# Kernel optimization log

Measured on AMD Instinct MI355X. Metric: run time of the kernel, lower is better.

## Reference

```python
import jax, jax.numpy as jnp
import numpy as np


def setup_inputs() -> dict:
    key = jax.random.key(0)
    ks = jax.random.split(key, 10)
    b, l, d, n, dc = 4, 4096, 768, 16, 4
    w = lambda k, shape, s: jax.random.normal(k, shape, jnp.float32) * s
    return {
        "x": w(ks[0], (b, l, d), 1.0),
        "state": jnp.zeros((b, d, n), jnp.float32),
        "W_in": w(ks[1], (d, 2 * d), 0.02),      # in_proj (expand_factor=2)
        "conv_w": w(ks[2], (d, dc), 0.1),          # depthwise conv1d weight [d_model, d_conv]
        "conv_b": w(ks[3], (d,), 0.02),
        "W_x": w(ks[4], (d, 2 * n), 0.02),         # x_proj -> (B, C)
        "W_dt": w(ks[5], (d, d), 0.02),
        "b_dt": w(ks[6], (d,), 0.02),
        "A_log": w(ks[7], (d, n), 0.1),
        "D": jnp.ones((d,), jnp.float32),
        "W_out": w(ks[8], (d, d), 0.02),
    }


def reference(x, state, W_in, conv_w, conv_b, W_x, W_dt, b_dt, A_log, D, W_out):
    b, l, d = x.shape
    n = A_log.shape[1]
    dc = conv_w.shape[1]

    xz = x @ W_in                              # [b,l,2d]
    x_ssm, z = jnp.split(xz, 2, axis=-1)       # each [b,l,d]

    # causal depthwise conv1d (torch pads by dc-1 both sides then truncates to l)
    xp = jnp.pad(x_ssm, ((0, 0), (dc - 1, 0), (0, 0)))
    x_conv = conv_b
    for k in range(dc):
        x_conv = x_conv + xp[:, k:k + l, :] * conv_w[:, k]
    x_ssm = jax.nn.silu(x_conv)

    A = -jnp.exp(A_log)                        # [d,n]
    dt = jax.nn.softplus(x_ssm @ W_dt + b_dt)  # [b,l,d]
    B_seq, C_seq = jnp.split(x_ssm @ W_x, 2, axis=-1)  # each [b,l,n]

    # selective scan: state[b,d,n] = state*exp(dt*A) + B*x ; y = <state,C> + D*x
    def step(s, inp):
        x_t, B_t, C_t, dt_t = inp              # [b,d],[b,n],[b,n],[b,d]
        dA = jnp.exp(dt_t[:, :, None] * A)     # [b,d,n]
        s = s * dA + B_t[:, None, :] * x_t[:, :, None]
        y = jnp.einsum('bdn,bn->bd', s, C_t) + D * x_t
        return s, y

    s0 = jnp.zeros((b, d, n), x.dtype)         # parallel_selective_scan starts from zeros
    _, ys = jax.lax.scan(
        step, s0,
        (x_ssm.transpose(1, 0, 2), B_seq.transpose(1, 0, 2),
         C_seq.transpose(1, 0, 2), dt.transpose(1, 0, 2)))
    y = ys.transpose(1, 0, 2)                  # [b,l,d]

    y = y * jax.nn.silu(z)
    out = y @ W_out
    # use_fused_ops path returns the (unchanged) incoming state as new_state
    return out, state
```

## Files before the change

kernel.cpp:

```cpp
#include <hip/hip_runtime.h>
#include <hip/hip_bf16.h>
#include <cstdint>
#include <cstddef>

constexpr int Bc = 4, Lc = 4096, Dc = 768, Nc = 16;
constexpr int M_TOT = Bc * Lc;
constexpr int NCH = 128;
constexpr int TCH = Lc / NCH;
constexpr int Kd = 768;
constexpr int TWO_D = 1536;

typedef __attribute__((ext_vector_type(8))) short short8v;
typedef __attribute__((ext_vector_type(4))) float f32x4;

__device__ __forceinline__ float fexp2(float x) {
#if __has_builtin(__builtin_amdgcn_exp2f)
    return __builtin_amdgcn_exp2f(x);
#else
    return exp2f(x);
#endif
}
__device__ __forceinline__ float softplusf(float x) {
    return (x > 20.0f) ? x : __logf(1.0f + __expf(x));
}
__device__ __forceinline__ float siluf(float x) {
    return x / (1.0f + __expf(-x));
}

__device__ __forceinline__ void swizzled_tile(int& row0, int& col0)
{
    const int nwg = gridDim.x * gridDim.y;
    const int bid = blockIdx.y * gridDim.x + blockIdx.x;
    const int swz = (bid & 7) * (nwg >> 3) + (bid >> 3);
    row0 = (swz / gridDim.x) * 128;
    col0 = (swz % gridDim.x) * 128;
}

__global__ __launch_bounds__(256)
void gemm_bf16_f32(const __hip_bfloat16* __restrict__ Ab,
                   const __hip_bfloat16* __restrict__ Wt,
                   int N, float* __restrict__ out0)
{
    __shared__ __hip_bfloat16 Asm[128 * 32];
    __shared__ __hip_bfloat16 Bsm[128 * 32];
    const int tid = threadIdx.x;
    const int w = tid >> 6, lane = tid & 63;
    const int lr = lane & 15, lc = lane >> 4;
    int row0, col0;
    swizzled_tile(row0, col0);
    const int wrow = (w >> 1) * 64, wcol = (w & 1) * 64;

    const int srow = lane >> 2;
    const int scol = (lane & 3) * 8;

    f32x4 acc[4][4] = {};

    const int KT = Kd / 32;
    for (int kt = 0; kt < KT; ++kt) {
        if (kt) __syncthreads();
        #pragma unroll
        for (int i = 0; i < 2; ++i) {
            const int seg = w * 2 + i;
            const __hip_bfloat16* asrc =
                Ab + (size_t)(row0 + seg * 16 + srow) * Kd + kt * 32 + scol;
            const __hip_bfloat16* bsrc =
                Wt + (size_t)(col0 + seg * 16 + srow) * Kd + kt * 32 + scol;
            __builtin_amdgcn_global_load_lds(
                (const __attribute__((address_space(1))) void*)asrc,
                (__attribute__((address_space(3))) void*)(Asm + seg * 512), 16, 0, 0);
            __builtin_amdgcn_global_load_lds(
                (const __attribute__((address_space(1))) void*)bsrc,
                (__attribute__((address_space(3))) void*)(Bsm + seg * 512), 16, 0, 0);
        }
        asm volatile("s_waitcnt vmcnt(0)" ::: "memory");
        __syncthreads();

        short8v a[4], b[4];
        #pragma unroll
        for (int m = 0; m < 4; ++m)
            a[m] = *(const short8v*)((char*)Asm + (wrow + m * 16 + lr) * 64 + lc * 16);
        #pragma unroll
        for (int nf = 0; nf < 4; ++nf)
            b[nf] = *(const short8v*)((char*)Bsm + (wcol + nf * 16 + lr) * 64 + lc * 16);
        #pragma unroll
        for (int m = 0; m < 4; ++m)
            #pragma unroll
            for (int nf = 0; nf < 4; ++nf)
                acc[m][nf] = __builtin_amdgcn_mfma_f32_16x16x32_bf16(
                    a[m], b[nf], acc[m][nf], 0, 0, 0);
    }

    #pragma unroll
    for (int m = 0; m < 4; ++m)
        #pragma unroll
        for (int nf = 0; nf < 4; ++nf)
            #pragma unroll
            for (int j = 0; j < 4; ++j) {
                const int rg = row0 + wrow + m * 16 + lc * 4 + j;
                const int cg = col0 + wcol + nf * 16 + lr;
                out0[(size_t)rg * N + cg] = acc[m][nf][j];
            }
}

__global__ __launch_bounds__(256)
void gemm_bf16_b16(const __hip_bfloat16* __restrict__ Ab,
                   const __hip_bfloat16* __restrict__ Wt,
                   int N, __hip_bfloat16* __restrict__ outb)
{
    __shared__ __hip_bfloat16 Asm[128 * 32];
    __shared__ __hip_bfloat16 Bsm[128 * 32];
    const int tid = threadIdx.x;
    const int w = tid >> 6, lane = tid & 63;
    const int lr = lane & 15, lc = lane >> 4;
    int row0, col0;
    swizzled_tile(row0, col0);
    const int wrow = (w >> 1) * 64, wcol = (w & 1) * 64;

    const int srow = lane >> 2;
    const int scol = (lane & 3) * 8;

    f32x4 acc[4][4] = {};

    const int KT = Kd / 32;
    for (int kt = 0; kt < KT; ++kt) {
        if (kt) __syncthreads();
        #pragma unroll
        for (int i = 0; i < 2; ++i) {
            const int seg = w * 2 + i;
            const __hip_bfloat16* asrc =
                Ab + (size_t)(row0 + seg * 16 + srow) * Kd + kt * 32 + scol;
            const __hip_bfloat16* bsrc =
                Wt + (size_t)(col0 + seg * 16 + srow) * Kd + kt * 32 + scol;
            __builtin_amdgcn_global_load_lds(
                (const __attribute__((address_space(1))) void*)asrc,
                (__attribute__((address_space(3))) void*)(Asm + seg * 512), 16, 0, 0);
            __builtin_amdgcn_global_load_lds(
                (const __attribute__((address_space(1))) void*)bsrc,
                (__attribute__((address_space(3))) void*)(Bsm + seg * 512), 16, 0, 0);
        }
        asm volatile("s_waitcnt vmcnt(0)" ::: "memory");
        __syncthreads();

        short8v a[4], b[4];
        #pragma unroll
        for (int m = 0; m < 4; ++m)
            a[m] = *(const short8v*)((char*)Asm + (wrow + m * 16 + lr) * 64 + lc * 16);
        #pragma unroll
        for (int nf = 0; nf < 4; ++nf)
            b[nf] = *(const short8v*)((char*)Bsm + (wcol + nf * 16 + lr) * 64 + lc * 16);
        #pragma unroll
        for (int m = 0; m < 4; ++m)
            #pragma unroll
            for (int nf = 0; nf < 4; ++nf)
                acc[m][nf] = __builtin_amdgcn_mfma_f32_16x16x32_bf16(
                    a[m], b[nf], acc[m][nf], 0, 0, 0);
    }

    #pragma unroll
    for (int m = 0; m < 4; ++m)
        #pragma unroll
        for (int nf = 0; nf < 4; ++nf)
            #pragma unroll
            for (int j = 0; j < 4; ++j) {
                const int rg = row0 + wrow + m * 16 + lc * 4 + j;
                const int cg = col0 + wcol + nf * 16 + lr;
                outb[(size_t)rg * N + cg] = __float2bfloat16(acc[m][nf][j]);
            }
}

__global__ __launch_bounds__(256)
void bc_mfma(const __hip_bfloat16* __restrict__ xsb,
             const __hip_bfloat16* __restrict__ WxT,
             float* __restrict__ BC)
{
    const int w = threadIdx.x >> 6, lane = threadIdx.x & 63;
    const int lr = lane & 15, lc = lane >> 4;
    const int row0 = blockIdx.x * 64 + w * 16;

    f32x4 acc0 = {}, acc1 = {};
    const __hip_bfloat16* ap = xsb + (size_t)(row0 + lr) * Kd + lc * 8;
    const __hip_bfloat16* b0p = WxT + (size_t)lr * Kd + lc * 8;
    const __hip_bfloat16* b1p = WxT + (size_t)(16 + lr) * Kd + lc * 8;
    #pragma unroll 4
    for (int kt = 0; kt < Kd / 32; ++kt) {
        const short8v a  = *(const short8v*)(ap  + kt * 32);
        const short8v b0 = *(const short8v*)(b0p + kt * 32);
        const short8v b1 = *(const short8v*)(b1p + kt * 32);
        acc0 = __builtin_amdgcn_mfma_f32_16x16x32_bf16(a, b0, acc0, 0, 0, 0);
        acc1 = __builtin_amdgcn_mfma_f32_16x16x32_bf16(a, b1, acc1, 0, 0, 0);
    }
    #pragma unroll
    for (int j = 0; j < 4; ++j) {
        const size_t r = (size_t)(row0 + lc * 4 + j) * 32;
        BC[r + lr]      = acc0[j];
        BC[r + 16 + lr] = acc1[j];
    }
}

__global__ __launch_bounds__(256)
void to_bf16_kernel(const float* __restrict__ src, __hip_bfloat16* __restrict__ dst, int n4)
{
    const int i = blockIdx.x * 256 + threadIdx.x;
    if (i >= n4) return;
    const float4 v = ((const float4*)src)[i];
    dst[i * 4 + 0] = __float2bfloat16(v.x);
    dst[i * 4 + 1] = __float2bfloat16(v.y);
    dst[i * 4 + 2] = __float2bfloat16(v.z);
    dst[i * 4 + 3] = __float2bfloat16(v.w);
}

__global__ __launch_bounds__(256)
void wtrans_kernel(const float* __restrict__ src, __hip_bfloat16* __restrict__ dst, int N)
{
    const int idx = blockIdx.x * 256 + threadIdx.x;
    if (idx >= N * Kd) return;
    const int n = idx / Kd, k = idx % Kd;
    dst[idx] = __float2bfloat16(src[(size_t)k * N + n]);
}

__global__ __launch_bounds__(256)
void aprep_kernel(const float* __restrict__ A_log, float* __restrict__ Abuf)
{
    const int i = blockIdx.x * 256 + threadIdx.x;
    if (i < Dc * Nc) Abuf[i] = -expf(A_log[i]) * 1.4426950408889634f;
}

__global__ __launch_bounds__(256)
void conv_silu_kernel(const __hip_bfloat16* __restrict__ xz16, const float* __restrict__ cw,
                      const float* __restrict__ cb, __hip_bfloat16* __restrict__ xsb)
{
    const int idx = blockIdx.x * 256 + threadIdx.x;
    if (idx >= (M_TOT / 8) * Dc) return;
    const int d = idx % Dc;
    const int r8 = idx / Dc;
    const int tb = r8 & (Lc / 8 - 1);
    const int b = r8 / (Lc / 8);
    const int t0 = tb * 8;
    const size_t rbase = (size_t)(b * Lc + t0);

    const float w0 = cw[d * 4 + 0], w1 = cw[d * 4 + 1];
    const float w2 = cw[d * 4 + 2], w3 = cw[d * 4 + 3];
    const float bias = cb[d];

    float xm3 = 0.f, xm2 = 0.f, xm1 = 0.f;
    if (t0 >= 3) {
        xm3 = __bfloat162float(xz16[(rbase - 3) * TWO_D + d]);
        xm2 = __bfloat162float(xz16[(rbase - 2) * TWO_D + d]);
        xm1 = __bfloat162float(xz16[(rbase - 1) * TWO_D + d]);
    }
    #pragma unroll
    for (int tt = 0; tt < 8; ++tt) {
        const float x0 = __bfloat162float(xz16[(rbase + tt) * TWO_D + d]);
        const float acc = fmaf(w3, x0, fmaf(w2, xm1, fmaf(w1, xm2, fmaf(w0, xm3, bias))));
        xsb[(rbase + tt) * Dc + d] = __float2bfloat16(siluf(acc));
        xm3 = xm2; xm2 = xm1; xm1 = x0;
    }
}

__global__ __launch_bounds__(256)
void scanA(const float* __restrict__ dtb, const __hip_bfloat16* __restrict__ xsb,
           const float* __restrict__ bc, const float* __restrict__ Abuf,
           const float* __restrict__ bdt,
           float* __restrict__ S, float* __restrict__ dcend)
{
    const int blk = blockIdx.x;
    const int dblk = blk % 3, ch = (blk / 3) % NCH, b = blk / (3 * NCH);
    const int d = dblk * 256 + threadIdx.x;
    const int t0 = ch * TCH;

    __shared__ float bcs[TCH * 32];
    {
        const int row = threadIdx.x >> 3, c4 = (threadIdx.x & 7) * 4;
        *(float4*)&bcs[row * 32 + c4] =
            *(const float4*)(bc + ((size_t)(b * Lc + t0) + row) * 32 + c4);
    }
    __syncthreads();

    float A[16];
    #pragma unroll
    for (int q = 0; q < 4; ++q)
        *(float4*)&A[q * 4] = *(const float4*)(Abuf + d * 16 + q * 4);
    const float bd = bdt[d];

    float s[16];
    #pragma unroll
    for (int n = 0; n < 16; ++n) s[n] = 0.f;

    const size_t base = ((size_t)(b * Lc + t0)) * Dc + d;
    float dc = 0.f;
    #pragma unroll 2
    for (int t = 0; t < TCH; ++t) {
        const float dt = softplusf(dtb[base + (size_t)t * Dc] + bd);
        const float x  = __bfloat162float(xsb[base + (size_t)t * Dc]);
        dc += dt;
        #pragma unroll
        for (int n = 0; n < 16; ++n) {
            const float dA = fexp2(dt * A[n]);
            s[n] = fmaf(s[n], dA, bcs[t * 32 + n] * x);
        }
    }
    const size_t g = (size_t)(b * NCH + ch) * Dc + d;
    #pragma unroll
    for (int n = 0; n < 16; ++n) S[g * 16 + n] = s[n];
    dcend[g] = dc;
}

__global__ __launch_bounds__(256)
void scanB(float* __restrict__ S_io, const float* __restrict__ dcend,
           const float* __restrict__ Abuf)
{
    const int tid = blockIdx.x * 256 + threadIdx.x;
    const int n = tid & 15;
    const int d = (tid >> 4) % Dc;
    const int b = tid / (16 * Dc);
    const float An = Abuf[d * 16 + n];
    float s = 0.f;
    for (int ch = 0; ch < NCH; ++ch) {
        const size_t g = (size_t)(b * NCH + ch) * Dc + d;
        const float sv = S_io[g * 16 + n];
        const float p  = fexp2(dcend[g] * An);
        S_io[g * 16 + n] = s;
        s = fmaf(s, p, sv);
    }
}

__global__ __launch_bounds__(256)
void scanC(const float* __restrict__ dtb, const __hip_bfloat16* __restrict__ xsb,
           const __hip_bfloat16* __restrict__ xz16, const float* __restrict__ bc,
           const float* __restrict__ Abuf, const float* __restrict__ bdt,
           const float* __restrict__ Ibuf, const float* __restrict__ Dvec,
           __hip_bfloat16* __restrict__ ybf)
{
    const int blk = blockIdx.x;
    const int dblk = blk % 3, ch = (blk / 3) % NCH, b = blk / (3 * NCH);
    const int d = dblk * 256 + threadIdx.x;
    const int t0 = ch * TCH;

    __shared__ float bcs[TCH * 32];
    {
        const int row = threadIdx.x >> 3, c4 = (threadIdx.x & 7) * 4;
        *(float4*)&bcs[row * 32 + c4] =
            *(const float4*)(bc + ((size_t)(b * Lc + t0) + row) * 32 + c4);
    }
    __syncthreads();

    float A[16], s[16];
    #pragma unroll
    for (int q = 0; q < 4; ++q)
        *(float4*)&A[q * 4] = *(const float4*)(Abuf + d * 16 + q * 4);
    const size_t g = (size_t)(b * NCH + ch) * Dc + d;
    #pragma unroll
    for (int q = 0; q < 4; ++q)
        *(float4*)&s[q * 4] = *(const float4*)(Ibuf + g * 16 + q * 4);
    const float bd = bdt[d];
    const float Dd = Dvec[d];

    const size_t base = ((size_t)(b * Lc + t0)) * Dc + d;
    const size_t zbase = ((size_t)(b * Lc + t0)) * TWO_D + Dc + d;
    #pragma unroll 2
    for (int t = 0; t < TCH; ++t) {
        const float dt = softplusf(dtb[base + (size_t)t * Dc] + bd);
        const float x  = __bfloat162float(xsb[base + (size_t)t * Dc]);
        const float z  = __bfloat162float(xz16[zbase + (size_t)t * TWO_D]);
        float yl = fmaf(Dd, x, 0.f);
        #pragma unroll
        for (int n = 0; n < 16; ++n) {
            const float dA = fexp2(dt * A[n]);
            s[n] = fmaf(s[n], dA, bcs[t * 32 + n] * x);
            yl = fmaf(s[n], bcs[t * 32 + 16 + n], yl);
        }
        ybf[base + (size_t)t * Dc] = __float2bfloat16(yl * siluf(z));
    }
}

extern "C" void kernel_launch(void* const* d_in, const int* in_sizes, int n_in,
                              void* d_out, int out_size, void* d_ws, size_t ws_size,
                              hipStream_t stream)
{
    const float* x      = (const float*)d_in[0];
    const float* state  = (const float*)d_in[1];
    const float* W_in   = (const float*)d_in[2];
    const float* conv_w = (const float*)d_in[3];
    const float* conv_b = (const float*)d_in[4];
    const float* W_x    = (const float*)d_in[5];
    const float* W_dt   = (const float*)d_in[6];
    const float* b_dt   = (const float*)d_in[7];
    const float* A_log  = (const float*)d_in[8];
    const float* Dvec   = (const float*)d_in[9];
    const float* W_out  = (const float*)d_in[10];
    float* out = (float*)d_out;

    char* wsb = (char*)d_ws;
    __hip_bfloat16* xz16 = (__hip_bfloat16*)wsb;     wsb += (size_t)M_TOT * TWO_D * 2;
    float* dtb   = (float*)wsb;                      wsb += (size_t)M_TOT * Dc * 4;
    float* bc    = (float*)wsb;                      wsb += (size_t)M_TOT * 32 * 4;
    float* Sb    = (float*)wsb;                      wsb += (size_t)Bc * NCH * Dc * Nc * 4;
    float* dcend = (float*)wsb;                      wsb += (size_t)Bc * NCH * Dc * 4;
    __hip_bfloat16* xb  = (__hip_bfloat16*)wsb;      wsb += (size_t)M_TOT * Dc * 2;
    __hip_bfloat16* xsb = (__hip_bfloat16*)wsb;      wsb += (size_t)M_TOT * Dc * 2;
    float* Abuf = (float*)wsb;                       wsb += (size_t)Dc * Nc * 4;
    __hip_bfloat16* WinT  = (__hip_bfloat16*)wsb;    wsb += (size_t)1536 * Kd * 2;
    __hip_bfloat16* WdtT  = (__hip_bfloat16*)wsb;    wsb += (size_t)768 * Kd * 2;
    __hip_bfloat16* WoutT = (__hip_bfloat16*)wsb;    wsb += (size_t)768 * Kd * 2;
    __hip_bfloat16* WxT   = (__hip_bfloat16*)wsb;    wsb += (size_t)32 * Kd * 2;
    float* Ib = Sb;
    __hip_bfloat16* ybf = xb;

    to_bf16_kernel<<<(M_TOT * Dc / 4 + 255) / 256, 256, 0, stream>>>(x, xb, M_TOT * Dc / 4);
    wtrans_kernel<<<(1536 * Kd + 255) / 256, 256, 0, stream>>>(W_in, WinT, 1536);
    wtrans_kernel<<<(768 * Kd + 255) / 256, 256, 0, stream>>>(W_dt, WdtT, 768);
    wtrans_kernel<<<(768 * Kd + 255) / 256, 256, 0, stream>>>(W_out, WoutT, 768);
    wtrans_kernel<<<(32 * Kd + 255) / 256, 256, 0, stream>>>(W_x, WxT, 32);
    aprep_kernel<<<(Dc * Nc + 255) / 256, 256, 0, stream>>>(A_log, Abuf);

    gemm_bf16_b16<<<dim3(TWO_D / 128, M_TOT / 128), 256, 0, stream>>>(
        xb, WinT, TWO_D, xz16);
    conv_silu_kernel<<<((M_TOT / 8) * Dc + 255) / 256, 256, 0, stream>>>(
        xz16, conv_w, conv_b, xsb);
    gemm_bf16_f32<<<dim3(Dc / 128, M_TOT / 128), 256, 0, stream>>>(xsb, WdtT, Dc, dtb);
    bc_mfma<<<M_TOT / 64, 256, 0, stream>>>(xsb, WxT, bc);
    scanA<<<Bc * NCH * 3, 256, 0, stream>>>(dtb, xsb, bc, Abuf, b_dt, Sb, dcend);
    scanB<<<(Bc * Dc * Nc) / 256, 256, 0, stream>>>(Sb, dcend, Abuf);
    scanC<<<Bc * NCH * 3, 256, 0, stream>>>(dtb, xsb, xz16, bc, Abuf, b_dt, Ib, Dvec, ybf);
    gemm_bf16_f32<<<dim3(Dc / 128, M_TOT / 128), 256, 0, stream>>>(ybf, WoutT, Dc, out);
    hipMemcpyAsync(out + (size_t)M_TOT * Dc, state,
                   (size_t)(Bc * Dc * Nc) * sizeof(float),
                   hipMemcpyDeviceToDevice, stream);
}
```

Before: 287.8 us.

## Fuse dt and B/C projections into one padded GEMM; tile weight transposes

```diff
diff --git a/kernel.cpp b/kernel.cpp
--- a/kernel.cpp
+++ b/kernel.cpp
@@ -9,6 +9,7 @@
 constexpr int TCH = Lc / NCH;
 constexpr int Kd = 768;
 constexpr int TWO_D = 1536;
+constexpr int NDTBC = 896;
 
 typedef __attribute__((ext_vector_type(8))) short short8v;
 typedef __attribute__((ext_vector_type(4))) float f32x4;
@@ -169,35 +170,6 @@
 }
 
 __global__ __launch_bounds__(256)
-void bc_mfma(const __hip_bfloat16* __restrict__ xsb,
-             const __hip_bfloat16* __restrict__ WxT,
-             float* __restrict__ BC)
-{
-    const int w = threadIdx.x >> 6, lane = threadIdx.x & 63;
-    const int lr = lane & 15, lc = lane >> 4;
-    const int row0 = blockIdx.x * 64 + w * 16;
-
-    f32x4 acc0 = {}, acc1 = {};
-    const __hip_bfloat16* ap = xsb + (size_t)(row0 + lr) * Kd + lc * 8;
-    const __hip_bfloat16* b0p = WxT + (size_t)lr * Kd + lc * 8;
-    const __hip_bfloat16* b1p = WxT + (size_t)(16 + lr) * Kd + lc * 8;
-    #pragma unroll 4
-    for (int kt = 0; kt < Kd / 32; ++kt) {
-        const short8v a  = *(const short8v*)(ap  + kt * 32);
-        const short8v b0 = *(const short8v*)(b0p + kt * 32);
-        const short8v b1 = *(const short8v*)(b1p + kt * 32);
-        acc0 = __builtin_amdgcn_mfma_f32_16x16x32_bf16(a, b0, acc0, 0, 0, 0);
-        acc1 = __builtin_amdgcn_mfma_f32_16x16x32_bf16(a, b1, acc1, 0, 0, 0);
-    }
-    #pragma unroll
-    for (int j = 0; j < 4; ++j) {
-        const size_t r = (size_t)(row0 + lc * 4 + j) * 32;
-        BC[r + lr]      = acc0[j];
-        BC[r + 16 + lr] = acc1[j];
-    }
-}
-
-__global__ __launch_bounds__(256)
 void to_bf16_kernel(const float* __restrict__ src, __hip_bfloat16* __restrict__ dst, int n4)
 {
     const int i = blockIdx.x * 256 + threadIdx.x;
@@ -210,12 +182,22 @@
 }
 
 __global__ __launch_bounds__(256)
-void wtrans_kernel(const float* __restrict__ src, __hip_bfloat16* __restrict__ dst, int N)
-{
-    const int idx = blockIdx.x * 256 + threadIdx.x;
-    if (idx >= N * Kd) return;
-    const int n = idx / Kd, k = idx % Kd;
-    dst[idx] = __float2bfloat16(src[(size_t)k * N + n]);
+void wtrans_tile(const float* __restrict__ src, __hip_bfloat16* __restrict__ dst, int N)
+{
+    __shared__ float tile[32][33];
+    const int n0 = blockIdx.x * 32, k0 = blockIdx.y * 32;
+    const int tx = threadIdx.x & 31, ty = threadIdx.x >> 5;
+    #pragma unroll
+    for (int r = 0; r < 4; ++r) {
+        const int k = ty + r * 8;
+        tile[k][tx] = src[(size_t)(k0 + k) * N + n0 + tx];
+    }
+    __syncthreads();
+    #pragma unroll
+    for (int r = 0; r < 4; ++r) {
+        const int n = ty + r * 8;
+        dst[(size_t)(n0 + n) * Kd + k0 + tx] = __float2bfloat16(tile[tx][n]);
+    }
 }
 
 __global__ __launch_bounds__(256)
@@ -258,21 +240,21 @@
 }
 
 __global__ __launch_bounds__(256)
-void scanA(const float* __restrict__ dtb, const __hip_bfloat16* __restrict__ xsb,
-           const float* __restrict__ bc, const float* __restrict__ Abuf,
-           const float* __restrict__ bdt,
+void scanA(const float* __restrict__ dtbc, const __hip_bfloat16* __restrict__ xsb,
+           const float* __restrict__ Abuf, const float* __restrict__ bdt,
            float* __restrict__ S, float* __restrict__ dcend)
 {
     const int blk = blockIdx.x;
     const int dblk = blk % 3, ch = (blk / 3) % NCH, b = blk / (3 * NCH);
     const int d = dblk * 256 + threadIdx.x;
     const int t0 = ch * TCH;
+    const size_t brow = (size_t)(b * Lc + t0);
 
     __shared__ float bcs[TCH * 32];
     {
         const int row = threadIdx.x >> 3, c4 = (threadIdx.x & 7) * 4;
         *(float4*)&bcs[row * 32 + c4] =
-            *(const float4*)(bc + ((size_t)(b * Lc + t0) + row) * 32 + c4);
+            *(const float4*)(dtbc + (brow + row) * NDTBC + Dc + c4);
     }
     __syncthreads();
 
@@ -286,17 +268,23 @@
     #pragma unroll
     for (int n = 0; n < 16; ++n) s[n] = 0.f;
 
-    const size_t base = ((size_t)(b * Lc + t0)) * Dc + d;
     float dc = 0.f;
     #pragma unroll 2
     for (int t = 0; t < TCH; ++t) {
-        const float dt = softplusf(dtb[base + (size_t)t * Dc] + bd);
-        const float x  = __bfloat162float(xsb[base + (size_t)t * Dc]);
+        const float dt = softplusf(dtbc[(brow + t) * NDTBC + d] + bd);
+        const float x  = __bfloat162float(xsb[(brow + t) * Dc + d]);
         dc += dt;
+        float Bt[16], Ct[16];
+        #pragma unroll
+        for (int q = 0; q < 4; ++q) {
+            *(float4*)&Bt[q * 4] = *(const float4*)&bcs[t * 32 + q * 4];
+            *(float4*)&Ct[q * 4] = *(const float4*)&bcs[t * 32 + 16 + q * 4];
+        }
+        (void)Ct;
         #pragma unroll
         for (int n = 0; n < 16; ++n) {
             const float dA = fexp2(dt * A[n]);
-            s[n] = fmaf(s[n], dA, bcs[t * 32 + n] * x);
+            s[n] = fmaf(s[n], dA, Bt[n] * x);
         }
     }
     const size_t g = (size_t)(b * NCH + ch) * Dc + d;
@@ -325,8 +313,8 @@
 }
 
 __global__ __launch_bounds__(256)
-void scanC(const float* __restrict__ dtb, const __hip_bfloat16* __restrict__ xsb,
-           const __hip_bfloat16* __restrict__ xz16, const float* __restrict__ bc,
+void scanC(const float* __restrict__ dtbc, const __hip_bfloat16* __restrict__ xsb,
+           const __hip_bfloat16* __restrict__ xz16,
            const float* __restrict__ Abuf, const float* __restrict__ bdt,
            const float* __restrict__ Ibuf, const float* __restrict__ Dvec,
            __hip_bfloat16* __restrict__ ybf)
@@ -335,12 +323,13 @@
     const int dblk = blk % 3, ch = (blk / 3) % NCH, b = blk / (3 * NCH);
     const int d = dblk * 256 + threadIdx.x;
     const int t0 = ch * TCH;
+    const size_t brow = (size_t)(b * Lc + t0);
 
     __shared__ float bcs[TCH * 32];
     {
         const int row = threadIdx.x >> 3, c4 = (threadIdx.x & 7) * 4;
         *(float4*)&bcs[row * 32 + c4] =
-            *(const float4*)(bc + ((size_t)(b * Lc + t0) + row) * 32 + c4);
+            *(const float4*)(dtbc + (brow + row) * NDTBC + Dc + c4);
     }
     __syncthreads();
 
@@ -355,21 +344,25 @@
     const float bd = bdt[d];
     const float Dd = Dvec[d];
 
-    const size_t base = ((size_t)(b * Lc + t0)) * Dc + d;
-    const size_t zbase = ((size_t)(b * Lc + t0)) * TWO_D + Dc + d;
     #pragma unroll 2
     for (int t = 0; t < TCH; ++t) {
-        const float dt = softplusf(dtb[base + (size_t)t * Dc] + bd);
-        const float x  = __bfloat162float(xsb[base + (size_t)t * Dc]);
-        const float z  = __bfloat162float(xz16[zbase + (size_t)t * TWO_D]);
+        const float dt = softplusf(dtbc[(brow + t) * NDTBC + d] + bd);
+        const float x  = __bfloat162float(xsb[(brow + t) * Dc + d]);
+        const float z  = __bfloat162float(xz16[(brow + t) * TWO_D + Dc + d]);
+        float Bt[16], Ct[16];
+        #pragma unroll
+        for (int q = 0; q < 4; ++q) {
+            *(float4*)&Bt[q * 4] = *(const float4*)&bcs[t * 32 + q * 4];
+            *(float4*)&Ct[q * 4] = *(const float4*)&bcs[t * 32 + 16 + q * 4];
+        }
         float yl = fmaf(Dd, x, 0.f);
         #pragma unroll
         for (int n = 0; n < 16; ++n) {
             const float dA = fexp2(dt * A[n]);
-            s[n] = fmaf(s[n], dA, bcs[t * 32 + n] * x);
-            yl = fmaf(s[n], bcs[t * 32 + 16 + n], yl);
-        }
-        ybf[base + (size_t)t * Dc] = __float2bfloat16(yl * siluf(z));
+            s[n] = fmaf(s[n], dA, Bt[n] * x);
+            yl = fmaf(s[n], Ct[n], yl);
+        }
+        ybf[(brow + t) * Dc + d] = __float2bfloat16(yl * siluf(z));
     }
 }
 
@@ -392,36 +385,34 @@
 
     char* wsb = (char*)d_ws;
     __hip_bfloat16* xz16 = (__hip_bfloat16*)wsb;     wsb += (size_t)M_TOT * TWO_D * 2;
-    float* dtb   = (float*)wsb;                      wsb += (size_t)M_TOT * Dc * 4;
-    float* bc    = (float*)wsb;                      wsb += (size_t)M_TOT * 32 * 4;
+    float* dtbc  = (float*)wsb;                      wsb += (size_t)M_TOT * NDTBC * 4;
     float* Sb    = (float*)wsb;                      wsb += (size_t)Bc * NCH * Dc * Nc * 4;
     float* dcend = (float*)wsb;                      wsb += (size_t)Bc * NCH * Dc * 4;
     __hip_bfloat16* xb  = (__hip_bfloat16*)wsb;      wsb += (size_t)M_TOT * Dc * 2;
     __hip_bfloat16* xsb = (__hip_bfloat16*)wsb;      wsb += (size_t)M_TOT * Dc * 2;
     float* Abuf = (float*)wsb;                       wsb += (size_t)Dc * Nc * 4;
     __hip_bfloat16* WinT  = (__hip_bfloat16*)wsb;    wsb += (size_t)1536 * Kd * 2;
-    __hip_bfloat16* WdtT  = (__hip_bfloat16*)wsb;    wsb += (size_t)768 * Kd * 2;
+    __hip_bfloat16* WcatT = (__hip_bfloat16*)wsb;    wsb += (size_t)NDTBC * Kd * 2;
     __hip_bfloat16* WoutT = (__hip_bfloat16*)wsb;    wsb += (size_t)768 * Kd * 2;
-    __hip_bfloat16* WxT   = (__hip_bfloat16*)wsb;    wsb += (size_t)32 * Kd * 2;
     float* Ib = Sb;
     __hip_bfloat16* ybf = xb;
 
     to_bf16_kernel<<<(M_TOT * Dc / 4 + 255) / 256, 256, 0, stream>>>(x, xb, M_TOT * Dc / 4);
-    wtrans_kernel<<<(1536 * Kd + 255) / 256, 256, 0, stream>>>(W_in, WinT, 1536);
-    wtrans_kernel<<<(768 * Kd + 255) / 256, 256, 0, stream>>>(W_dt, WdtT, 768);
-    wtrans_kernel<<<(768 * Kd + 255) / 256, 256, 0, stream>>>(W_out, WoutT, 768);
-    wtrans_kernel<<<(32 * Kd + 255) / 256, 256, 0, stream>>>(W_x, WxT, 32);
+    wtrans_tile<<<dim3(1536 / 32, Kd / 32), 256, 0, stream>>>(W_in, WinT, 1536);
+    wtrans_tile<<<dim3(768 / 32, Kd / 32), 256, 0, stream>>>(W_dt, WcatT, 768);
+    wtrans_tile<<<dim3(32 / 32, Kd / 32), 256, 0, stream>>>(W_x, WcatT + (size_t)768 * Kd, 32);
+    wtrans_tile<<<dim3(768 / 32, Kd / 32), 256, 0, stream>>>(W_out, WoutT, 768);
     aprep_kernel<<<(Dc * Nc + 255) / 256, 256, 0, stream>>>(A_log, Abuf);
 
     gemm_bf16_b16<<<dim3(TWO_D / 128, M_TOT / 128), 256, 0, stream>>>(
         xb, WinT, TWO_D, xz16);
     conv_silu_kernel<<<((M_TOT / 8) * Dc + 255) / 256, 256, 0, stream>>>(
         xz16, conv_w, conv_b, xsb);
-    gemm_bf16_f32<<<dim3(Dc / 128, M_TOT / 128), 256, 0, stream>>>(xsb, WdtT, Dc, dtb);
-    bc_mfma<<<M_TOT / 64, 256, 0, stream>>>(xsb, WxT, bc);
-    scanA<<<Bc * NCH * 3, 256, 0, stream>>>(dtb, xsb, bc, Abuf, b_dt, Sb, dcend);
+    gemm_bf16_f32<<<dim3(NDTBC / 128, M_TOT / 128), 256, 0, stream>>>(
+        xsb, WcatT, NDTBC, dtbc);
+    scanA<<<Bc * NCH * 3, 256, 0, stream>>>(dtbc, xsb, Abuf, b_dt, Sb, dcend);
     scanB<<<(Bc * Dc * Nc) / 256, 256, 0, stream>>>(Sb, dcend, Abuf);
-    scanC<<<Bc * NCH * 3, 256, 0, stream>>>(dtb, xsb, xz16, bc, Abuf, b_dt, Ib, Dvec, ybf);
+    scanC<<<Bc * NCH * 3, 256, 0, stream>>>(dtbc, xsb, xz16, Abuf, b_dt, Ib, Dvec, ybf);
     gemm_bf16_f32<<<dim3(Dc / 128, M_TOT / 128), 256, 0, stream>>>(ybf, WoutT, Dc, out);
     hipMemcpyAsync(out + (size_t)M_TOT * Dc, state,
                    (size_t)(Bc * Dc * Nc) * sizeof(float),
```

Measured after the change: 278.6 us. 3.2% less time.
